# Performance work log

Hardware: AMD Instinct MI355X
Metric: run time of the kernel (lower is better)

The kernel has to match this reference:

```python
import jax, jax.numpy as jnp
import numpy as np

NUM_HEADS = 8
EPS = 1e-12  # matches torch F.normalize default eps


def setup_inputs() -> dict:
    key = jax.random.key(0)
    k1, k2 = jax.random.split(key)
    x = jax.random.normal(k1, (8, 384, 128, 128), dtype=jnp.float32)
    # 1x1 conv weight [out=3*dim, in=dim]
    w_qkv = jax.random.normal(k2, (1152, 384), dtype=jnp.float32) * (1.0 / np.sqrt(384))
    return {"x": x, "w_qkv": w_qkv}


def _l2norm(t):
    # torch F.normalize(dim=-1): x / max(||x||2, eps)
    n = jnp.sqrt(jnp.sum(t * t, axis=-1, keepdims=True))
    return t / jnp.maximum(n, EPS)


def reference(x, w_qkv):
    B, C, H, W = x.shape
    hw = H * W
    head_c = C // NUM_HEADS
    # 1x1 conv == channel matmul
    qkv = jnp.einsum('bchw,oc->bohw', x, w_qkv)  # [B, 3C, H, W]
    q, k, v = jnp.split(qkv, 3, axis=1)
    def rs(t):
        return t.reshape(B, NUM_HEADS, head_c, hw)
    q, k, v = rs(q), rs(k), rs(v)
    q = _l2norm(q)
    k = _l2norm(k)
    scale = jnp.sqrt(jnp.float32(hw))
    attn = jnp.einsum('bhcn,bhdn->bhcd', q, k) / scale  # small CxC per head
    attn = jax.nn.softmax(attn, axis=-1)
    out = jnp.einsum('bhcd,bhdn->bhcn', attn, v)
    return out.reshape(B, C, H, W)
```

## Files before the change

kernel.cpp:

```cpp
#include <hip/hip_runtime.h>

typedef short short8 __attribute__((ext_vector_type(8)));
typedef __bf16 bf16x8 __attribute__((ext_vector_type(8)));
typedef float f32x4 __attribute__((ext_vector_type(4)));
typedef int i32x4 __attribute__((ext_vector_type(4)));

typedef const __attribute__((address_space(1))) void* gas_p;
typedef __attribute__((address_space(3))) void* las_p;

static __device__ __forceinline__ unsigned short f2bf(float f) {
  unsigned u = __builtin_bit_cast(unsigned, f);
  u += 0x7fffu + ((u >> 16) & 1u);
  return (unsigned short)(u >> 16);
}
static __device__ __forceinline__ float bf2f(unsigned short h) {
  unsigned u = ((unsigned)h) << 16;
  return __builtin_bit_cast(float, u);
}

#define MFMA16(a, b, c) __builtin_amdgcn_mfma_f32_16x16x32_bf16( \
    __builtin_bit_cast(bf16x8, a), __builtin_bit_cast(bf16x8, b), (c), 0, 0, 0)

__global__ __launch_bounds__(64) void k0_wfrag(const float* __restrict__ w,
                                               unsigned short* __restrict__ wfrag) {
  int bx = blockIdx.x;
  int m16 = bx / 12, kb = bx % 12;
  int lane = threadIdx.x;
  int i = lane & 15, g = lane >> 4;
  int o = m16 * 16 + i;
  int k = kb * 32 + g * 8;
  const float* src = w + (size_t)o * 384 + k;
  f32x4 f0 = *(const f32x4*)(src);
  f32x4 f1 = *(const f32x4*)(src + 4);
  short8 v;
#pragma unroll
  for (int j = 0; j < 4; ++j) { v[j] = (short)f2bf(f0[j]); v[4 + j] = (short)f2bf(f1[j]); }
  *(short8*)(wfrag + ((size_t)(m16 * 12 + kb) * 64 + lane) * 8) = v;
}

__global__ __launch_bounds__(256) void kx_transpose(const float* __restrict__ x,
                                                    unsigned short* __restrict__ xt,
                                                    int bbase) {
  __shared__ unsigned T[64 * 32];
  int n0 = blockIdx.x * 64, c0 = blockIdx.y * 64;
  int bl = blockIdx.z;
  int bg = bbase + bl;
  int t = threadIdx.x;
  int cl2 = t >> 6, nl = t & 63;
  const float* xb = x + ((size_t)bg * 384 + c0) * 16384 + n0 + nl;
#pragma unroll
  for (int u = 0; u < 8; ++u) {
    int cb = cl2 * 2 + u * 8;
    float f0 = xb[(size_t)cb * 16384];
    float f1 = xb[(size_t)(cb + 1) * 16384];
    unsigned p = (unsigned)f2bf(f0) | ((unsigned)f2bf(f1) << 16);
    int cp = cb >> 1;
    T[nl * 32 + (cp ^ (nl & 31))] = p;
  }
  __syncthreads();
  int nl2 = t >> 2, cg = t & 3;
  unsigned vals[8];
#pragma unroll
  for (int j = 0; j < 8; ++j)
    vals[j] = T[nl2 * 32 + ((cg * 8 + j) ^ (nl2 & 31))];
  unsigned short* dst = xt + ((size_t)bl * 16384 + n0 + nl2) * 384 + c0 + cg * 16;
  *(i32x4*)(dst)     = (i32x4){(int)vals[0], (int)vals[1], (int)vals[2], (int)vals[3]};
  *(i32x4*)(dst + 8) = (i32x4){(int)vals[4], (int)vals[5], (int)vals[6], (int)vals[7]};
}

__global__ __launch_bounds__(256, 4) void k1_qkv(const unsigned short* __restrict__ xt,
                                                 const unsigned short* __restrict__ wfrag,
                                                 unsigned short* __restrict__ qkv,
                                                 float* __restrict__ norms2,
                                                 int bbase, int nb) {
  __shared__ union {
    unsigned short Bt[2][128 * 32];
    unsigned short Cl[128 * 136];
  } sm;

  int flat = blockIdx.x;
  int b_l = flat % nb;
  int rem = flat / nb;
  int m = rem % 9, ntile = rem / 9;
  int o0 = m * 128, n0 = ntile * 128;
  int bg = bbase + b_l;
  int t = threadIdx.x;
  int wave = t >> 6, lane = t & 63;
  int i = lane & 15, g = lane >> 4;
  int mh = wave >> 1, nh = wave & 1;

  int r = t >> 2, blk = t & 3;
  int srcblk = blk ^ (r & 3);
  const unsigned short* xrow =
      xt + ((size_t)b_l * 16384 + n0 + r) * 384 + srcblk * 8;

  const unsigned short* wbase = wfrag + ((size_t)(m * 8 + mh * 4) * 12 * 64 + lane) * 8;

  f32x4 acc[4][4];
#pragma unroll
  for (int a = 0; a < 4; ++a)
#pragma unroll
    for (int c = 0; c < 4; ++c) acc[a][c] = (f32x4){0.f, 0.f, 0.f, 0.f};

#define STAGE(buf, kb)                                                          \
  do {                                                                          \
    const unsigned short* s0 = xrow + (kb) * 32;                                \
    unsigned short* d0 = &sm.Bt[0][0] + (buf) * 4096 + t * 8;                   \
    __builtin_amdgcn_global_load_lds((gas_p)s0, (las_p)d0, 16, 0, 0);           \
    __builtin_amdgcn_global_load_lds((gas_p)(s0 + (size_t)64 * 384),            \
                                     (las_p)(d0 + 2048), 16, 0, 0);             \
  } while (0)

  short8 aF[4];
#pragma unroll
  for (int mt = 0; mt < 4; ++mt)
    aF[mt] = *(const short8*)(wbase + (size_t)(mt * 12) * 512);
  STAGE(0, 0);

  for (int kb = 0; kb < 12; ++kb) {
    __syncthreads();
    if (kb < 11) STAGE((kb + 1) & 1, kb + 1);
    const unsigned short* bb = &sm.Bt[kb & 1][0];
    int swz = (g ^ (i & 3)) * 8;
#pragma unroll
    for (int nt = 0; nt < 4; ++nt) {
      short8 bF = *(const short8*)(bb + (nh * 64 + nt * 16 + i) * 32 + swz);
#pragma unroll
      for (int mt = 0; mt < 4; ++mt) acc[mt][nt] = MFMA16(aF[mt], bF, acc[mt][nt]);
    }
    if (kb < 11) {
#pragma unroll
      for (int mt = 0; mt < 4; ++mt)
        aF[mt] = *(const short8*)(wbase + (size_t)(mt * 12 + kb + 1) * 512);
    }
  }
#undef STAGE

  __syncthreads();

#pragma unroll
  for (int mt = 0; mt < 4; ++mt)
#pragma unroll
    for (int nt = 0; nt < 4; ++nt)
#pragma unroll
      for (int rr = 0; rr < 4; ++rr)
        sm.Cl[(mh * 64 + mt * 16 + 4 * g + rr) * 136 + nh * 64 + nt * 16 + i] =
            f2bf(acc[mt][nt][rr]);
  __syncthreads();

  size_t obase = ((size_t)bg * 1152 + o0) * 16384 + n0;
  int srow = t >> 4, scol = (t & 15) * 8;
#pragma unroll
  for (int u = 0; u < 8; ++u) {
    int row = u * 16 + srow;
    short8 vv = *(const short8*)&sm.Cl[row * 136 + scol];
    *(short8*)(qkv + obase + (size_t)row * 16384 + scol) = vv;
  }

  if (o0 < 768) {
    int row = t >> 1, half = t & 1;
    const unsigned short* p = &sm.Cl[row * 136 + half * 64];
    float s = 0.f;
#pragma unroll
    for (int u = 0; u < 8; ++u) {
      short8 vv = *(const short8*)(p + u * 8);
#pragma unroll
      for (int e = 0; e < 8; ++e) {
        float f = bf2f((unsigned short)vv[e]);
        s += f * f;
      }
    }
    s += __shfl_xor(s, 1, 64);
    if (half == 0) atomicAdd(&norms2[bg * 768 + o0 + row], s);
  }
}

__global__ __launch_bounds__(256) void k2_gram(const unsigned short* __restrict__ qkv,
                                               float* __restrict__ G) {
  __shared__ unsigned short Bt[2][96 * 128];
  __shared__ float Gl[48 * 48];
  int bh = blockIdx.x >> 4, chunk = blockIdx.x & 15;
  int b = bh >> 3, hi = bh & 7;
  int t = threadIdx.x, wave = t >> 6, lane = t & 63;
  int i = lane & 15, g = lane >> 4;

  for (int u = t; u < 2304; u += 256) Gl[u] = 0.f;

  const unsigned short* qrow = qkv + ((size_t)b * 1152 + hi * 48) * 16384;
  const unsigned short* krow = qrow + (size_t)384 * 16384;
  int P = chunk * 1024;

  int srow = t >> 4;
  int sblk = (t & 15) ^ (srow & 7);

#define STAGE2(buf, tt)                                                         \
  do {                                                                          \
    int p0 = P + (tt) * 128 + sblk * 8;                                         \
    unsigned short* d0 = &Bt[buf][0] + t * 8;                                   \
    _Pragma("unroll")                                                           \
    for (int e = 0; e < 3; ++e) {                                               \
      __builtin_amdgcn_global_load_lds(                                         \
          (gas_p)(qrow + (size_t)(e * 16 + srow) * 16384 + p0),                 \
          (las_p)(d0 + e * 2048), 16, 0, 0);                                    \
      __builtin_amdgcn_global_load_lds(                                         \
          (gas_p)(krow + (size_t)(e * 16 + srow) * 16384 + p0),                 \
          (las_p)(d0 + (e + 3) * 2048), 16, 0, 0);                              \
    }                                                                           \
  } while (0)

  f32x4 acc[3][3];
#pragma unroll
  for (int a = 0; a < 3; ++a)
#pragma unroll
    for (int c = 0; c < 3; ++c) acc[a][c] = (f32x4){0.f, 0.f, 0.f, 0.f};

  STAGE2(0, 0);
  int ksg = wave * 4 + g;
  for (int tt = 0; tt < 8; ++tt) {
    __syncthreads();
    if (tt < 7) STAGE2((tt + 1) & 1, tt + 1);
    const unsigned short* bb = &Bt[tt & 1][0];
    int d = (ksg ^ (i & 7)) * 8;
    short8 aF[3], bF[3];
#pragma unroll
    for (int mt = 0; mt < 3; ++mt)
      aF[mt] = *(const short8*)(bb + (mt * 16 + i) * 128 + d);
#pragma unroll
    for (int nt = 0; nt < 3; ++nt)
      bF[nt] = *(const short8*)(bb + (48 + nt * 16 + i) * 128 + d);
#pragma unroll
    for (int mt = 0; mt < 3; ++mt)
#pragma unroll
      for (int nt = 0; nt < 3; ++nt) acc[mt][nt] = MFMA16(aF[mt], bF[nt], acc[mt][nt]);
  }
#undef STAGE2

  __syncthreads();
#pragma unroll
  for (int mt = 0; mt < 3; ++mt)
#pragma unroll
    for (int nt = 0; nt < 3; ++nt)
#pragma unroll
      for (int rr = 0; rr < 4; ++rr)
        atomicAdd(&Gl[(mt * 16 + 4 * g + rr) * 48 + nt * 16 + i], acc[mt][nt][rr]);
  __syncthreads();
  float* Gg = G + (size_t)bh * 2304;
  for (int u = t; u < 2304; u += 256) atomicAdd(&Gg[u], Gl[u]);
}

__global__ __launch_bounds__(64) void k2b_softmax(const float* __restrict__ G,
                                                  const float* __restrict__ norms2,
                                                  float* __restrict__ attn) {
  int bh = blockIdx.x;
  int b = bh >> 3, hi = bh & 7;
  int c = threadIdx.x;
  if (c >= 48) return;
  const float* Gg = G + (size_t)bh * 2304 + c * 48;
  const float* nq = norms2 + b * 768 + hi * 48;
  const float* nk = nq + 384;
  float dq = fmaxf(sqrtf(nq[c]), 1e-12f);
  float l[48];
  float m = -1e30f;
#pragma unroll
  for (int d = 0; d < 48; ++d) {
    float dk = fmaxf(sqrtf(nk[d]), 1e-12f);
    l[d] = Gg[d] / (dq * dk * 128.0f);
    m = fmaxf(m, l[d]);
  }
  float s = 0.f;
#pragma unroll
  for (int d = 0; d < 48; ++d) {
    l[d] = expf(l[d] - m);
    s += l[d];
  }
  float inv = 1.0f / s;
  float* A = attn + (size_t)bh * 2304 + c * 48;
#pragma unroll
  for (int d = 0; d < 48; ++d) A[d] = l[d] * inv;
}

__global__ __launch_bounds__(256) void k3_out(const unsigned short* __restrict__ qkv,
                                              const float* __restrict__ attn,
                                              float* __restrict__ out) {
  __shared__ unsigned short Vt[256 * 72];
  int nchunk = blockIdx.x, bh = blockIdx.y;
  int b = bh >> 3, hi = bh & 7;
  int n0 = nchunk * 256;
  int t = threadIdx.x, wave = t >> 6, lane = t & 63;
  int i = lane & 15, g = lane >> 4;

  const unsigned short* vbase = qkv + ((size_t)b * 1152 + 768 + hi * 48) * 16384 + n0 + t;
  unsigned short* vr = &Vt[t * 72];
#pragma unroll
  for (int dp = 0; dp < 24; ++dp) {
    unsigned a0 = vbase[(size_t)(2 * dp) * 16384];
    unsigned a1 = vbase[(size_t)(2 * dp + 1) * 16384];
    *(unsigned*)(vr + 2 * dp) = a0 | (a1 << 16);
  }
  *(i32x4*)(vr + 48) = (i32x4){0, 0, 0, 0};
  *(i32x4*)(vr + 56) = (i32x4){0, 0, 0, 0};

  const float* Ab = attn + (size_t)bh * 2304;
  short8 aF[3][2];
#pragma unroll
  for (int mt = 0; mt < 3; ++mt) {
    int row = mt * 16 + i;
    f32x4 f0 = *(const f32x4*)(Ab + row * 48 + 8 * g);
    f32x4 f1 = *(const f32x4*)(Ab + row * 48 + 8 * g + 4);
    short8 a0;
#pragma unroll
    for (int j = 0; j < 4; ++j) { a0[j] = (short)f2bf(f0[j]); a0[4 + j] = (short)f2bf(f1[j]); }
    aF[mt][0] = a0;
    short8 a1v = (short8){0, 0, 0, 0, 0, 0, 0, 0};
    if (g < 2) {
      f32x4 h0 = *(const f32x4*)(Ab + row * 48 + 32 + 8 * g);
      f32x4 h1 = *(const f32x4*)(Ab + row * 48 + 32 + 8 * g + 4);
#pragma unroll
      for (int j = 0; j < 4; ++j) { a1v[j] = (short)f2bf(h0[j]); a1v[4 + j] = (short)f2bf(h1[j]); }
    }
    aF[mt][1] = a1v;
  }
  __syncthreads();

  f32x4 acc[3][4];
#pragma unroll
  for (int a = 0; a < 3; ++a)
#pragma unroll
    for (int c = 0; c < 4; ++c) acc[a][c] = (f32x4){0.f, 0.f, 0.f, 0.f};

  int nb = wave * 64;
#pragma unroll
  for (int nt = 0; nt < 4; ++nt) {
    const unsigned short* vp = &Vt[(size_t)(nb + nt * 16 + i) * 72 + 8 * g];
    short8 b0 = *(const short8*)vp;
    short8 b1 = *(const short8*)(vp + 32);
#pragma unroll
    for (int mt = 0; mt < 3; ++mt) {
      acc[mt][nt] = MFMA16(aF[mt][0], b0, acc[mt][nt]);
      acc[mt][nt] = MFMA16(aF[mt][1], b1, acc[mt][nt]);
    }
  }

  float* ob = out + ((size_t)b * 384 + hi * 48) * 16384 + n0 + nb;
#pragma unroll
  for (int mt = 0; mt < 3; ++mt)
#pragma unroll
    for (int nt = 0; nt < 4; ++nt)
#pragma unroll
      for (int rr = 0; rr < 4; ++rr)
        ob[(size_t)(mt * 16 + 4 * g + rr) * 16384 + nt * 16 + i] = acc[mt][nt][rr];
}

extern "C" void kernel_launch(void* const* d_in, const int* in_sizes, int n_in,
                              void* d_out, int out_size, void* d_ws, size_t ws_size,
                              hipStream_t stream) {
  const float* x = (const float*)d_in[0];
  const float* w = (const float*)d_in[1];
  float* out = (float*)d_out;
  char* ws = (char*)d_ws;

  unsigned short* qkv   = (unsigned short*)(ws);
  unsigned short* wfrag = (unsigned short*)(ws + 301989888LL);
  float* norms2         = (float*)(ws + 302874624LL);
  float* G              = (float*)(ws + 302899200LL);
  float* attn           = (float*)(ws + 303489024LL);
  unsigned short* xtb   = (unsigned short*)(ws + 304078848LL);

  const size_t FULL_NEED = 304078848LL + 100663296LL;

  hipMemsetAsync(ws + 302874624LL, 0, 24576 + 589824, stream);
  k0_wfrag<<<864, 64, 0, stream>>>(w, wfrag);

  if (ws_size >= FULL_NEED) {
    kx_transpose<<<dim3(256, 6, 8), 256, 0, stream>>>(x, xtb, 0);
    k1_qkv<<<9216, 256, 0, stream>>>(xtb, wfrag, qkv, norms2, 0, 8);
  } else {
    for (int b = 0; b < 8; ++b) {
      kx_transpose<<<dim3(256, 6, 1), 256, 0, stream>>>(x, xtb, b);
      k1_qkv<<<1152, 256, 0, stream>>>(xtb, wfrag, qkv, norms2, b, 1);
    }
  }

  k2_gram<<<1024, 256, 0, stream>>>(qkv, G);
  k2b_softmax<<<64, 64, 0, stream>>>(G, norms2, attn);
  k3_out<<<dim3(64, 64), 256, 0, stream>>>(qkv, attn, out);
}
```

Baseline: 392.2 us.

## Widen QKV k-step to 64, halve gram blocks, replace global atomics with partial sums

The QKV GEMM now stages 64-wide K slices (6 steps instead of 12) with an 8-way XOR swizzle, which halves the barrier count per block at the cost of twice the LDS. The gram kernel covers 2048 positions per block across 512 blocks and writes per-chunk partial Gram matrices into reused workspace instead of issuing global atomics. The softmax kernel sums the eight partials in shared memory first. This drops the memset of G and the global atomic traffic, but LDS use rises, which may reduce occupancy in k1.

Result: slower. 477.7 us (+21.8%).

```diff
diff --git a/kernel.cpp b/kernel.cpp
--- a/kernel.cpp
+++ b/kernel.cpp
@@ -74,7 +74,7 @@
                                                  float* __restrict__ norms2,
                                                  int bbase, int nb) {
   __shared__ union {
-    unsigned short Bt[2][128 * 32];
+    unsigned short Bt[2][128 * 64];
     unsigned short Cl[128 * 136];
   } sm;
 
@@ -89,52 +89,60 @@
   int i = lane & 15, g = lane >> 4;
   int mh = wave >> 1, nh = wave & 1;
 
-  int r = t >> 2, blk = t & 3;
-  int srcblk = blk ^ (r & 3);
+  int nloc = t >> 3;
+  int sblk = (t & 7) ^ (nloc & 7);
   const unsigned short* xrow =
-      xt + ((size_t)b_l * 16384 + n0 + r) * 384 + srcblk * 8;
+      xt + ((size_t)b_l * 16384 + n0 + nloc) * 384 + sblk * 8;
 
   const unsigned short* wbase = wfrag + ((size_t)(m * 8 + mh * 4) * 12 * 64 + lane) * 8;
 
+#define STG(buf, step)                                                        \
+  do {                                                                        \
+    _Pragma("unroll")                                                         \
+    for (int e = 0; e < 4; ++e)                                               \
+      __builtin_amdgcn_global_load_lds(                                       \
+          (gas_p)(xrow + (size_t)(e * 32) * 384 + (step) * 64),               \
+          (las_p)(&sm.Bt[buf][(e * 256 + t) * 8]), 16, 0, 0);                 \
+  } while (0)
+
   f32x4 acc[4][4];
 #pragma unroll
   for (int a = 0; a < 4; ++a)
 #pragma unroll
     for (int c = 0; c < 4; ++c) acc[a][c] = (f32x4){0.f, 0.f, 0.f, 0.f};
 
-#define STAGE(buf, kb)                                                          \
-  do {                                                                          \
-    const unsigned short* s0 = xrow + (kb) * 32;                                \
-    unsigned short* d0 = &sm.Bt[0][0] + (buf) * 4096 + t * 8;                   \
-    __builtin_amdgcn_global_load_lds((gas_p)s0, (las_p)d0, 16, 0, 0);           \
-    __builtin_amdgcn_global_load_lds((gas_p)(s0 + (size_t)64 * 384),            \
-                                     (las_p)(d0 + 2048), 16, 0, 0);             \
-  } while (0)
-
-  short8 aF[4];
-#pragma unroll
-  for (int mt = 0; mt < 4; ++mt)
-    aF[mt] = *(const short8*)(wbase + (size_t)(mt * 12) * 512);
-  STAGE(0, 0);
-
-  for (int kb = 0; kb < 12; ++kb) {
+  short8 aF[2][4];
+#pragma unroll
+  for (int kk = 0; kk < 2; ++kk)
+#pragma unroll
+    for (int mt = 0; mt < 4; ++mt)
+      aF[kk][mt] = *(const short8*)(wbase + (size_t)(mt * 12 + kk) * 512);
+  STG(0, 0);
+
+  for (int st = 0; st < 6; ++st) {
     __syncthreads();
-    if (kb < 11) STAGE((kb + 1) & 1, kb + 1);
-    const unsigned short* bb = &sm.Bt[kb & 1][0];
-    int swz = (g ^ (i & 3)) * 8;
-#pragma unroll
-    for (int nt = 0; nt < 4; ++nt) {
-      short8 bF = *(const short8*)(bb + (nh * 64 + nt * 16 + i) * 32 + swz);
-#pragma unroll
-      for (int mt = 0; mt < 4; ++mt) acc[mt][nt] = MFMA16(aF[mt], bF, acc[mt][nt]);
-    }
-    if (kb < 11) {
-#pragma unroll
-      for (int mt = 0; mt < 4; ++mt)
-        aF[mt] = *(const short8*)(wbase + (size_t)(mt * 12 + kb + 1) * 512);
-    }
-  }
-#undef STAGE
+    if (st < 5) STG((st + 1) & 1, st + 1);
+    const unsigned short* bb = &sm.Bt[st & 1][0];
+#pragma unroll
+    for (int kk = 0; kk < 2; ++kk) {
+#pragma unroll
+      for (int nt = 0; nt < 4; ++nt) {
+        int n = nh * 64 + nt * 16 + i;
+        short8 bF = *(const short8*)(bb + n * 64 + ((kk * 4 + g) ^ (n & 7)) * 8);
+#pragma unroll
+        for (int mt = 0; mt < 4; ++mt) acc[mt][nt] = MFMA16(aF[kk][mt], bF, acc[mt][nt]);
+      }
+    }
+    if (st < 5) {
+#pragma unroll
+      for (int kk = 0; kk < 2; ++kk)
+#pragma unroll
+        for (int mt = 0; mt < 4; ++mt)
+          aF[kk][mt] =
+              *(const short8*)(wbase + (size_t)(mt * 12 + (st + 1) * 2 + kk) * 512);
+    }
+  }
+#undef STG
 
   __syncthreads();
 
@@ -176,19 +184,19 @@
 }
 
 __global__ __launch_bounds__(256) void k2_gram(const unsigned short* __restrict__ qkv,
-                                               float* __restrict__ G) {
-  __shared__ unsigned short Bt[2][96 * 128];
-  __shared__ float Gl[48 * 48];
-  int bh = blockIdx.x >> 4, chunk = blockIdx.x & 15;
+                                               float* __restrict__ Gpart) {
+  __shared__ union {
+    unsigned short Bt[2][96 * 128];
+    float Gl[48 * 48];
+  } sm;
+  int bh = blockIdx.x >> 3, chunk = blockIdx.x & 7;
   int b = bh >> 3, hi = bh & 7;
   int t = threadIdx.x, wave = t >> 6, lane = t & 63;
   int i = lane & 15, g = lane >> 4;
 
-  for (int u = t; u < 2304; u += 256) Gl[u] = 0.f;
-
   const unsigned short* qrow = qkv + ((size_t)b * 1152 + hi * 48) * 16384;
   const unsigned short* krow = qrow + (size_t)384 * 16384;
-  int P = chunk * 1024;
+  int P = chunk * 2048;
 
   int srow = t >> 4;
   int sblk = (t & 15) ^ (srow & 7);
@@ -196,7 +204,7 @@
 #define STAGE2(buf, tt)                                                         \
   do {                                                                          \
     int p0 = P + (tt) * 128 + sblk * 8;                                         \
-    unsigned short* d0 = &Bt[buf][0] + t * 8;                                   \
+    unsigned short* d0 = &sm.Bt[buf][0] + t * 8;                                \
     _Pragma("unroll")                                                           \
     for (int e = 0; e < 3; ++e) {                                               \
       __builtin_amdgcn_global_load_lds(                                         \
@@ -216,10 +224,10 @@
 
   STAGE2(0, 0);
   int ksg = wave * 4 + g;
-  for (int tt = 0; tt < 8; ++tt) {
+  for (int tt = 0; tt < 16; ++tt) {
     __syncthreads();
-    if (tt < 7) STAGE2((tt + 1) & 1, tt + 1);
-    const unsigned short* bb = &Bt[tt & 1][0];
+    if (tt < 15) STAGE2((tt + 1) & 1, tt + 1);
+    const unsigned short* bb = &sm.Bt[tt & 1][0];
     int d = (ksg ^ (i & 7)) * 8;
     short8 aF[3], bF[3];
 #pragma unroll
@@ -236,26 +244,38 @@
 #undef STAGE2
 
   __syncthreads();
+  for (int u = t; u < 2304; u += 256) sm.Gl[u] = 0.f;
+  __syncthreads();
 #pragma unroll
   for (int mt = 0; mt < 3; ++mt)
 #pragma unroll
     for (int nt = 0; nt < 3; ++nt)
 #pragma unroll
       for (int rr = 0; rr < 4; ++rr)
-        atomicAdd(&Gl[(mt * 16 + 4 * g + rr) * 48 + nt * 16 + i], acc[mt][nt][rr]);
-  __syncthreads();
-  float* Gg = G + (size_t)bh * 2304;
-  for (int u = t; u < 2304; u += 256) atomicAdd(&Gg[u], Gl[u]);
-}
-
-__global__ __launch_bounds__(64) void k2b_softmax(const float* __restrict__ G,
-                                                  const float* __restrict__ norms2,
-                                                  float* __restrict__ attn) {
+        atomicAdd(&sm.Gl[(mt * 16 + 4 * g + rr) * 48 + nt * 16 + i],
+                  acc[mt][nt][rr]);
+  __syncthreads();
+  float* Gg = Gpart + (size_t)(bh * 8 + chunk) * 2304;
+  for (int u = t; u < 2304; u += 256) Gg[u] = sm.Gl[u];
+}
+
+__global__ __launch_bounds__(256) void k2b_softmax(const float* __restrict__ Gpart,
+                                                   const float* __restrict__ norms2,
+                                                   float* __restrict__ attn) {
+  __shared__ float Gl[2304];
   int bh = blockIdx.x;
   int b = bh >> 3, hi = bh & 7;
-  int c = threadIdx.x;
-  if (c >= 48) return;
-  const float* Gg = G + (size_t)bh * 2304 + c * 48;
+  int t = threadIdx.x;
+  const float* base = Gpart + (size_t)bh * 8 * 2304;
+  for (int u = t; u < 2304; u += 256) {
+    float s = 0.f;
+#pragma unroll
+    for (int ch = 0; ch < 8; ++ch) s += base[(size_t)ch * 2304 + u];
+    Gl[u] = s;
+  }
+  __syncthreads();
+  if (t >= 48) return;
+  int c = t;
   const float* nq = norms2 + b * 768 + hi * 48;
   const float* nk = nq + 384;
   float dq = fmaxf(sqrtf(nq[c]), 1e-12f);
@@ -264,7 +284,7 @@
 #pragma unroll
   for (int d = 0; d < 48; ++d) {
     float dk = fmaxf(sqrtf(nk[d]), 1e-12f);
-    l[d] = Gg[d] / (dq * dk * 128.0f);
+    l[d] = Gl[c * 48 + d] / (dq * dk * 128.0f);
     m = fmaxf(m, l[d]);
   }
   float s = 0.f;
@@ -362,13 +382,13 @@
   unsigned short* qkv   = (unsigned short*)(ws);
   unsigned short* wfrag = (unsigned short*)(ws + 301989888LL);
   float* norms2         = (float*)(ws + 302874624LL);
-  float* G              = (float*)(ws + 302899200LL);
   float* attn           = (float*)(ws + 303489024LL);
   unsigned short* xtb   = (unsigned short*)(ws + 304078848LL);
+  float* Gpart          = (float*)xtb;
 
   const size_t FULL_NEED = 304078848LL + 100663296LL;
 
-  hipMemsetAsync(ws + 302874624LL, 0, 24576 + 589824, stream);
+  hipMemsetAsync(ws + 302874624LL, 0, 24576, stream);
   k0_wfrag<<<864, 64, 0, stream>>>(w, wfrag);
 
   if (ws_size >= FULL_NEED) {
@@ -381,7 +401,7 @@
     }
   }
 
-  k2_gram<<<1024, 256, 0, stream>>>(qkv, G);
-  k2b_softmax<<<64, 64, 0, stream>>>(G, norms2, attn);
+  k2_gram<<<512, 256, 0, stream>>>(qkv, Gpart);
+  k2b_softmax<<<64, 256, 0, stream>>>(Gpart, norms2, attn);
   k3_out<<<dim3(64, 64), 256, 0, stream>>>(qkv, attn, out);
 }
```
